# Performance work log

Hardware: AMD Instinct MI355X
Metric: run time of the kernel (lower is better)

Reference implementation:

```python
import jax, jax.numpy as jnp
import numpy as np

DIM = 1024
NUM_EXPERTS = 8
ACTIVE_EXPERTS = 2
EXPERT_DIM = 2048


def setup_inputs() -> dict:
    key = jax.random.key(0)
    k1, k2, k3, k4 = jax.random.split(key, 4)
    x = jax.random.normal(k1, (1, 2048, DIM), dtype=jnp.float32)
    gate_w = jax.random.normal(k2, (NUM_EXPERTS, DIM), dtype=jnp.float32) * 0.02
    balance_bias = jnp.zeros((NUM_EXPERTS,), dtype=jnp.float32)
    w1 = jax.random.normal(k3, (NUM_EXPERTS, EXPERT_DIM, DIM), dtype=jnp.float32) * 0.02
    w2 = jax.random.normal(k4, (NUM_EXPERTS, DIM, EXPERT_DIM), dtype=jnp.float32) * 0.02
    return {"x": x, "gate_w": gate_w, "balance_bias": balance_bias, "w1": w1, "w2": w2}


def reference(x, gate_w, balance_bias, w1, w2):
    B, S, D = x.shape
    T = B * S
    xf = x.reshape(T, D)
    # gating: sigmoid scores with load-balance bias, then top-k
    gate_logits = jnp.einsum('td,ed->te', xf, gate_w)
    gate_scores = jax.nn.sigmoid(gate_logits + balance_bias)
    topk_scores, topk_idx = jax.lax.top_k(gate_scores, ACTIVE_EXPERTS)
    topk_scores = topk_scores / (topk_scores.sum(axis=-1, keepdims=True) + 1e-6)
    # scatter normalized scores into dense combine weights [T, E]
    comb = jnp.zeros((T, NUM_EXPERTS), dtype=x.dtype)
    comb = comb.at[jnp.arange(T)[:, None], topk_idx].add(topk_scores)
    # expert FFNs (dense over experts; combine weight zeroes unselected)
    h = jax.nn.silu(jnp.einsum('td,ehd->teh', xf, w1))   # [T, E, expert_dim]
    expert_out = jnp.einsum('teh,edh->ted', h, w2)        # [T, E, D]
    out = jnp.einsum('te,ted->td', comb, expert_out)
    return out.reshape(B, S, D)
```

## Files before the change

kernel.cpp:

```cpp
#include <hip/hip_runtime.h>

#define T 2048
#define DIM 1024
#define NE 8
#define ED 2048
#define NSLOT (T * 2)
#define KSPLIT 2

#define BM 128
#define BN 128
#define BK 32

typedef __attribute__((ext_vector_type(8))) short s8v;
typedef __attribute__((ext_vector_type(4))) float f32x4;

__device__ __forceinline__ short f2bf(float f) {
    union { float f; unsigned u; } v;
    v.f = f;
    unsigned r = 0x7FFFu + ((v.u >> 16) & 1u);
    v.u += r;
    return (short)(v.u >> 16);
}

__device__ __forceinline__ float bf2f(short s) {
    union { unsigned u; float f; } v;
    v.u = ((unsigned)(unsigned short)s) << 16;
    return v.f;
}

__global__ void router_kernel(const float* __restrict__ x,
                              const float* __restrict__ gw,
                              const float* __restrict__ bias,
                              short* __restrict__ xb,
                              int* __restrict__ counts,
                              int* __restrict__ top2i,
                              float* __restrict__ top2w) {
    int wid = threadIdx.x >> 6;
    int lane = threadIdx.x & 63;
    int t = blockIdx.x * 4 + wid;

    const float* xr = x + (size_t)t * DIM + lane * 16;
    float4 xv[4];
#pragma unroll
    for (int j = 0; j < 4; ++j) xv[j] = *(const float4*)(xr + j * 4);

    s8v o0, o1;
#pragma unroll
    for (int j = 0; j < 2; ++j) {
        o0[j * 4 + 0] = f2bf(xv[j].x); o0[j * 4 + 1] = f2bf(xv[j].y);
        o0[j * 4 + 2] = f2bf(xv[j].z); o0[j * 4 + 3] = f2bf(xv[j].w);
        o1[j * 4 + 0] = f2bf(xv[j + 2].x); o1[j * 4 + 1] = f2bf(xv[j + 2].y);
        o1[j * 4 + 2] = f2bf(xv[j + 2].z); o1[j * 4 + 3] = f2bf(xv[j + 2].w);
    }
    *(s8v*)(xb + (size_t)t * DIM + lane * 16) = o0;
    *(s8v*)(xb + (size_t)t * DIM + lane * 16 + 8) = o1;

    float sc[NE];
#pragma unroll
    for (int e = 0; e < NE; ++e) {
        const float* gr = gw + e * DIM + lane * 16;
        float p = 0.f;
#pragma unroll
        for (int j = 0; j < 4; ++j) {
            float4 g = *(const float4*)(gr + j * 4);
            p += xv[j].x * g.x + xv[j].y * g.y + xv[j].z * g.z + xv[j].w * g.w;
        }
#pragma unroll
        for (int off = 32; off; off >>= 1) p += __shfl_xor(p, off, 64);
        sc[e] = 1.f / (1.f + __expf(-(p + bias[e])));
    }
    int b0 = 0; float s0 = sc[0];
#pragma unroll
    for (int e = 1; e < NE; ++e) if (sc[e] > s0) { s0 = sc[e]; b0 = e; }
    int b1 = -1; float s1 = -1e30f;
#pragma unroll
    for (int e = 0; e < NE; ++e) if (e != b0 && sc[e] > s1) { s1 = sc[e]; b1 = e; }
    float inv = 1.f / (s0 + s1 + 1e-6f);
    if (lane == 0) {
        top2i[t * 2 + 0] = b0; top2i[t * 2 + 1] = b1;
        top2w[t * 2 + 0] = s0 * inv; top2w[t * 2 + 1] = s1 * inv;
        atomicAdd(&counts[b0], 1);
        atomicAdd(&counts[b1], 1);
    }
}

__global__ void prefix_kernel(const int* __restrict__ counts, int* __restrict__ offsets) {
    if (threadIdx.x == 0) {
        int a = 0;
        for (int e = 0; e < NE; ++e) { offsets[e] = a; a += counts[e]; }
    }
}

__global__ void scatter_kernel(const int* __restrict__ top2i,
                               const int* __restrict__ offsets, int* __restrict__ running,
                               int* __restrict__ tok_list, int* __restrict__ slot_of) {
    int t = blockIdx.x * blockDim.x + threadIdx.x;
    if (t >= T) return;
#pragma unroll
    for (int k = 0; k < 2; ++k) {
        int e = top2i[t * 2 + k];
        int pos = atomicAdd(&running[e], 1);
        int slot = offsets[e] + pos;
        tok_list[slot] = t;
        slot_of[t * 2 + k] = slot;
    }
}

__global__ __launch_bounds__(256) void ffn1_kernel(
    const short* __restrict__ xb, const float* __restrict__ w1,
    const int* __restrict__ counts, const int* __restrict__ offsets,
    const int* __restrict__ tok_list, short* __restrict__ h) {
    int e = blockIdx.z;
    int cnt = counts[e];
    int m0 = blockIdx.y * BM;
    if (m0 >= cnt) return;
    int off = offsets[e];
    int n0 = blockIdx.x * BN;

    __shared__ __align__(16) short As[4][BM][8];
    __shared__ __align__(16) short Bs[4][BN][8];

    int tid = threadIdx.x;
    int lane = tid & 63, wid = tid >> 6;
    int mo = (wid >> 1) * 64, no = (wid & 1) * 64;
    int lrow = lane & 15, lq = lane >> 4;

    f32x4 acc[4][4];
#pragma unroll
    for (int mi = 0; mi < 4; ++mi)
#pragma unroll
        for (int ni = 0; ni < 4; ++ni) acc[mi][ni] = (f32x4){0.f, 0.f, 0.f, 0.f};

    int r0 = tid >> 2, q0 = tid & 3;
    int rm0 = m0 + r0;      if (rm0 > cnt - 1) rm0 = cnt - 1;
    int rm1 = m0 + r0 + 64; if (rm1 > cnt - 1) rm1 = cnt - 1;
    int tk0 = tok_list[off + rm0];
    int tk1 = tok_list[off + rm1];
    const short* a0p = xb + (size_t)tk0 * DIM + q0 * 8;
    const short* a1p = xb + (size_t)tk1 * DIM + q0 * 8;
    const float* wb0 = w1 + ((size_t)e * ED + n0 + r0) * DIM + q0 * 8;
    const float* wb1 = wb0 + (size_t)64 * DIM;

    for (int k0 = 0; k0 < DIM; k0 += BK) {
        s8v av0 = *(const s8v*)(a0p + k0);
        s8v av1 = *(const s8v*)(a1p + k0);
        float4 f00 = *(const float4*)(wb0 + k0);
        float4 f01 = *(const float4*)(wb0 + k0 + 4);
        float4 f10 = *(const float4*)(wb1 + k0);
        float4 f11 = *(const float4*)(wb1 + k0 + 4);
        s8v bv0 = { f2bf(f00.x), f2bf(f00.y), f2bf(f00.z), f2bf(f00.w),
                    f2bf(f01.x), f2bf(f01.y), f2bf(f01.z), f2bf(f01.w) };
        s8v bv1 = { f2bf(f10.x), f2bf(f10.y), f2bf(f10.z), f2bf(f10.w),
                    f2bf(f11.x), f2bf(f11.y), f2bf(f11.z), f2bf(f11.w) };
        __syncthreads();
        *(s8v*)&As[q0][r0][0] = av0;
        *(s8v*)&As[q0][r0 + 64][0] = av1;
        *(s8v*)&Bs[q0][r0][0] = bv0;
        *(s8v*)&Bs[q0][r0 + 64][0] = bv1;
        __syncthreads();
        s8v af[4], bf[4];
#pragma unroll
        for (int mi = 0; mi < 4; ++mi) af[mi] = *(const s8v*)&As[lq][mo + mi * 16 + lrow][0];
#pragma unroll
        for (int ni = 0; ni < 4; ++ni) bf[ni] = *(const s8v*)&Bs[lq][no + ni * 16 + lrow][0];
#pragma unroll
        for (int mi = 0; mi < 4; ++mi)
#pragma unroll
            for (int ni = 0; ni < 4; ++ni)
                acc[mi][ni] = __builtin_amdgcn_mfma_f32_16x16x32_bf16(af[mi], bf[ni], acc[mi][ni], 0, 0, 0);
    }

#pragma unroll
    for (int mi = 0; mi < 4; ++mi) {
#pragma unroll
        for (int ni = 0; ni < 4; ++ni) {
            int ln = n0 + no + ni * 16 + lrow;
#pragma unroll
            for (int r = 0; r < 4; ++r) {
                int row = m0 + mo + mi * 16 + lq * 4 + r;
                if (row < cnt) {
                    float v = acc[mi][ni][r];
                    v = v / (1.f + __expf(-v));
                    h[(size_t)(off + row) * ED + ln] = f2bf(v);
                }
            }
        }
    }
}

__global__ __launch_bounds__(256) void ffn2_kernel(
    const short* __restrict__ h, const float* __restrict__ w2,
    const int* __restrict__ counts, const int* __restrict__ offsets,
    short* __restrict__ eo) {
    int z = blockIdx.z;
    int e = z >> 1, ks = z & 1;
    int cnt = counts[e];
    int m0 = blockIdx.y * BM;
    if (m0 >= cnt) return;
    int off = offsets[e];
    int n0 = blockIdx.x * BN;
    const int kbase = ks * (ED / KSPLIT);

    __shared__ __align__(16) short As[4][BM][8];
    __shared__ __align__(16) short Bs[4][BN][8];

    int tid = threadIdx.x;
    int lane = tid & 63, wid = tid >> 6;
    int mo = (wid >> 1) * 64, no = (wid & 1) * 64;
    int lrow = lane & 15, lq = lane >> 4;

    f32x4 acc[4][4];
#pragma unroll
    for (int mi = 0; mi < 4; ++mi)
#pragma unroll
        for (int ni = 0; ni < 4; ++ni) acc[mi][ni] = (f32x4){0.f, 0.f, 0.f, 0.f};

    int r0 = tid >> 2, q0 = tid & 3;
    int rm0 = m0 + r0;      if (rm0 > cnt - 1) rm0 = cnt - 1;
    int rm1 = m0 + r0 + 64; if (rm1 > cnt - 1) rm1 = cnt - 1;
    const short* a0p = h + (size_t)(off + rm0) * ED + q0 * 8;
    const short* a1p = h + (size_t)(off + rm1) * ED + q0 * 8;
    const float* wb0 = w2 + ((size_t)e * DIM + n0 + r0) * ED + q0 * 8;
    const float* wb1 = wb0 + (size_t)64 * ED;

    for (int k0 = kbase; k0 < kbase + ED / KSPLIT; k0 += BK) {
        s8v av0 = *(const s8v*)(a0p + k0);
        s8v av1 = *(const s8v*)(a1p + k0);
        float4 f00 = *(const float4*)(wb0 + k0);
        float4 f01 = *(const float4*)(wb0 + k0 + 4);
        float4 f10 = *(const float4*)(wb1 + k0);
        float4 f11 = *(const float4*)(wb1 + k0 + 4);
        s8v bv0 = { f2bf(f00.x), f2bf(f00.y), f2bf(f00.z), f2bf(f00.w),
                    f2bf(f01.x), f2bf(f01.y), f2bf(f01.z), f2bf(f01.w) };
        s8v bv1 = { f2bf(f10.x), f2bf(f10.y), f2bf(f10.z), f2bf(f10.w),
                    f2bf(f11.x), f2bf(f11.y), f2bf(f11.z), f2bf(f11.w) };
        __syncthreads();
        *(s8v*)&As[q0][r0][0] = av0;
        *(s8v*)&As[q0][r0 + 64][0] = av1;
        *(s8v*)&Bs[q0][r0][0] = bv0;
        *(s8v*)&Bs[q0][r0 + 64][0] = bv1;
        __syncthreads();
        s8v af[4], bf[4];
#pragma unroll
        for (int mi = 0; mi < 4; ++mi) af[mi] = *(const s8v*)&As[lq][mo + mi * 16 + lrow][0];
#pragma unroll
        for (int ni = 0; ni < 4; ++ni) bf[ni] = *(const s8v*)&Bs[lq][no + ni * 16 + lrow][0];
#pragma unroll
        for (int mi = 0; mi < 4; ++mi)
#pragma unroll
            for (int ni = 0; ni < 4; ++ni)
                acc[mi][ni] = __builtin_amdgcn_mfma_f32_16x16x32_bf16(af[mi], bf[ni], acc[mi][ni], 0, 0, 0);
    }

    short* eop = eo + (size_t)ks * NSLOT * DIM;
#pragma unroll
    for (int mi = 0; mi < 4; ++mi) {
#pragma unroll
        for (int ni = 0; ni < 4; ++ni) {
            int ln = n0 + no + ni * 16 + lrow;
#pragma unroll
            for (int r = 0; r < 4; ++r) {
                int row = m0 + mo + mi * 16 + lq * 4 + r;
                if (row < cnt) {
                    eop[(size_t)(off + row) * DIM + ln] = f2bf(acc[mi][ni][r]);
                }
            }
        }
    }
}

__global__ __launch_bounds__(256) void combine_kernel(
    const short* __restrict__ eo, const int* __restrict__ slot_of,
    const float* __restrict__ top2w, float* __restrict__ out) {
    int idx = blockIdx.x * 256 + threadIdx.x;
    int t = idx >> 7;
    int c = idx & 127;
    int s0 = slot_of[2 * t], s1 = slot_of[2 * t + 1];
    float w0 = top2w[2 * t], w1 = top2w[2 * t + 1];
    const short* e0 = eo;
    const short* e1 = eo + (size_t)NSLOT * DIM;
    s8v a0 = *(const s8v*)(e0 + (size_t)s0 * DIM + c * 8);
    s8v a1 = *(const s8v*)(e1 + (size_t)s0 * DIM + c * 8);
    s8v b0 = *(const s8v*)(e0 + (size_t)s1 * DIM + c * 8);
    s8v b1 = *(const s8v*)(e1 + (size_t)s1 * DIM + c * 8);
    float4 o[2];
#pragma unroll
    for (int j = 0; j < 8; ++j) {
        float v = w0 * (bf2f(a0[j]) + bf2f(a1[j])) + w1 * (bf2f(b0[j]) + bf2f(b1[j]));
        ((float*)o)[j] = v;
    }
    float4* op = (float4*)(out + (size_t)t * DIM + c * 8);
    op[0] = o[0];
    op[1] = o[1];
}

extern "C" void kernel_launch(void* const* d_in, const int* in_sizes, int n_in,
                              void* d_out, int out_size, void* d_ws, size_t ws_size,
                              hipStream_t stream) {
    const float* x    = (const float*)d_in[0];
    const float* gw   = (const float*)d_in[1];
    const float* bias = (const float*)d_in[2];
    const float* w1   = (const float*)d_in[3];
    const float* w2   = (const float*)d_in[4];
    float* out = (float*)d_out;

    char* ws = (char*)d_ws;
    short* xb = (short*)ws;
    short* h  = (short*)(ws + (4u << 20));
    short* eo = (short*)(ws + (20u << 20));
    char* meta = ws + (36u << 20);
    int*   counts   = (int*)(meta);
    int*   running  = (int*)(meta + 32);
    int*   offsets  = (int*)(meta + 64);
    int*   tok_list = (int*)(meta + 96);
    int*   slot_of  = (int*)(meta + 96 + 4 * NSLOT);
    int*   top2i    = (int*)(meta + 96 + 8 * NSLOT);
    float* top2w    = (float*)(meta + 96 + 8 * NSLOT + 8 * T);

    hipMemsetAsync(meta, 0, 64, stream);

    router_kernel<<<T / 4, 256, 0, stream>>>(x, gw, bias, xb, counts, top2i, top2w);
    prefix_kernel<<<1, 64, 0, stream>>>(counts, offsets);
    scatter_kernel<<<8, 256, 0, stream>>>(top2i, offsets, running, tok_list, slot_of);
    ffn1_kernel<<<dim3(ED / BN, T / BM, NE), 256, 0, stream>>>(xb, w1, counts, offsets, tok_list, h);
    ffn2_kernel<<<dim3(DIM / BN, T / BM, NE * KSPLIT), 256, 0, stream>>>(h, w2, counts, offsets, eo);
    combine_kernel<<<T * DIM / 8 / 256, 256, 0, stream>>>(eo, slot_of, top2w, out);
}
```

Before: 336.3 us.

## Pre-convert expert weights to bf16 and load GEMM tiles directly into LDS

A new kernel converts w1 and w2 from fp32 to bf16 into workspace at the start of each call. The FFN GEMMs then stream bf16 tiles straight into shared memory with global_load_lds, which removes the per-tile fp32 loads, in-loop conversion and register staging. The prefix and scatter kernels are merged into one single-block plan kernel that uses shared-memory atomics. The trade-off is an extra full pass over both weight tensors, reading fp32 and writing bf16, on every call. The LDS loads are still not double-buffered.

```diff
diff --git a/kernel.cpp b/kernel.cpp
--- a/kernel.cpp
+++ b/kernel.cpp
@@ -6,6 +6,7 @@
 #define ED 2048
 #define NSLOT (T * 2)
 #define KSPLIT 2
+#define WTOT (NE * ED * DIM)
 
 #define BM 128
 #define BN 128
@@ -26,6 +27,30 @@
     union { unsigned u; float f; } v;
     v.u = ((unsigned)(unsigned short)s) << 16;
     return v.f;
+}
+
+__device__ __forceinline__ void glds16(const void* g, void* l) {
+    __builtin_amdgcn_global_load_lds(
+        (const __attribute__((address_space(1))) void*)g,
+        (__attribute__((address_space(3))) void*)l, 16, 0, 0);
+}
+
+__global__ __launch_bounds__(256) void convert_w_kernel(
+    const float* __restrict__ w1, const float* __restrict__ w2,
+    short* __restrict__ w1b, short* __restrict__ w2b) {
+    size_t c = (size_t)blockIdx.x * 256 + threadIdx.x;
+    const float* p1 = w1 + c * 8;
+    const float* p2 = w2 + c * 8;
+    float4 a0 = *(const float4*)(p1);
+    float4 a1 = *(const float4*)(p1 + 4);
+    float4 b0 = *(const float4*)(p2);
+    float4 b1 = *(const float4*)(p2 + 4);
+    s8v o1 = { f2bf(a0.x), f2bf(a0.y), f2bf(a0.z), f2bf(a0.w),
+               f2bf(a1.x), f2bf(a1.y), f2bf(a1.z), f2bf(a1.w) };
+    s8v o2 = { f2bf(b0.x), f2bf(b0.y), f2bf(b0.z), f2bf(b0.w),
+               f2bf(b1.x), f2bf(b1.y), f2bf(b1.z), f2bf(b1.w) };
+    *(s8v*)(w1b + c * 8) = o1;
+    *(s8v*)(w2b + c * 8) = o2;
 }
 
 __global__ void router_kernel(const float* __restrict__ x,
@@ -84,30 +109,30 @@
     }
 }
 
-__global__ void prefix_kernel(const int* __restrict__ counts, int* __restrict__ offsets) {
+__global__ __launch_bounds__(256) void plan_kernel(
+    const int* __restrict__ counts, const int* __restrict__ top2i,
+    int* __restrict__ offsets, int* __restrict__ tok_list, int* __restrict__ slot_of) {
+    __shared__ int soff[NE];
+    __shared__ int srun[NE];
     if (threadIdx.x == 0) {
         int a = 0;
-        for (int e = 0; e < NE; ++e) { offsets[e] = a; a += counts[e]; }
-    }
-}
-
-__global__ void scatter_kernel(const int* __restrict__ top2i,
-                               const int* __restrict__ offsets, int* __restrict__ running,
-                               int* __restrict__ tok_list, int* __restrict__ slot_of) {
-    int t = blockIdx.x * blockDim.x + threadIdx.x;
-    if (t >= T) return;
-#pragma unroll
-    for (int k = 0; k < 2; ++k) {
-        int e = top2i[t * 2 + k];
-        int pos = atomicAdd(&running[e], 1);
-        int slot = offsets[e] + pos;
-        tok_list[slot] = t;
-        slot_of[t * 2 + k] = slot;
+        for (int e = 0; e < NE; ++e) { soff[e] = a; offsets[e] = a; a += counts[e]; srun[e] = 0; }
+    }
+    __syncthreads();
+    for (int t = threadIdx.x; t < T; t += 256) {
+#pragma unroll
+        for (int k = 0; k < 2; ++k) {
+            int e = top2i[t * 2 + k];
+            int pos = atomicAdd(&srun[e], 1);
+            int slot = soff[e] + pos;
+            tok_list[slot] = t;
+            slot_of[t * 2 + k] = slot;
+        }
     }
 }
 
 __global__ __launch_bounds__(256) void ffn1_kernel(
-    const short* __restrict__ xb, const float* __restrict__ w1,
+    const short* __restrict__ xb, const short* __restrict__ w1b,
     const int* __restrict__ counts, const int* __restrict__ offsets,
     const int* __restrict__ tok_list, short* __restrict__ h) {
     int e = blockIdx.z;
@@ -121,8 +146,8 @@
     __shared__ __align__(16) short Bs[4][BN][8];
 
     int tid = threadIdx.x;
-    int lane = tid & 63, wid = tid >> 6;
-    int mo = (wid >> 1) * 64, no = (wid & 1) * 64;
+    int lane = tid & 63, w = tid >> 6;
+    int mo = (w >> 1) * 64, no = (w & 1) * 64;
     int lrow = lane & 15, lq = lane >> 4;
 
     f32x4 acc[4][4];
@@ -131,32 +156,23 @@
 #pragma unroll
         for (int ni = 0; ni < 4; ++ni) acc[mi][ni] = (f32x4){0.f, 0.f, 0.f, 0.f};
 
-    int r0 = tid >> 2, q0 = tid & 3;
-    int rm0 = m0 + r0;      if (rm0 > cnt - 1) rm0 = cnt - 1;
-    int rm1 = m0 + r0 + 64; if (rm1 > cnt - 1) rm1 = cnt - 1;
-    int tk0 = tok_list[off + rm0];
-    int tk1 = tok_list[off + rm1];
-    const short* a0p = xb + (size_t)tk0 * DIM + q0 * 8;
-    const short* a1p = xb + (size_t)tk1 * DIM + q0 * 8;
-    const float* wb0 = w1 + ((size_t)e * ED + n0 + r0) * DIM + q0 * 8;
-    const float* wb1 = wb0 + (size_t)64 * DIM;
+    int ra0 = m0 + lane;      if (ra0 > cnt - 1) ra0 = cnt - 1;
+    int ra1 = m0 + 64 + lane; if (ra1 > cnt - 1) ra1 = cnt - 1;
+    const short* a0 = xb + (size_t)tok_list[off + ra0] * DIM + w * 8;
+    const short* a1 = xb + (size_t)tok_list[off + ra1] * DIM + w * 8;
+    const short* b0 = w1b + ((size_t)e * ED + n0 + lane) * DIM + w * 8;
+    const short* b1 = b0 + (size_t)64 * DIM;
+    short* lA0 = &As[w][0][0];
+    short* lA1 = &As[w][64][0];
+    short* lB0 = &Bs[w][0][0];
+    short* lB1 = &Bs[w][64][0];
 
     for (int k0 = 0; k0 < DIM; k0 += BK) {
-        s8v av0 = *(const s8v*)(a0p + k0);
-        s8v av1 = *(const s8v*)(a1p + k0);
-        float4 f00 = *(const float4*)(wb0 + k0);
-        float4 f01 = *(const float4*)(wb0 + k0 + 4);
-        float4 f10 = *(const float4*)(wb1 + k0);
-        float4 f11 = *(const float4*)(wb1 + k0 + 4);
-        s8v bv0 = { f2bf(f00.x), f2bf(f00.y), f2bf(f00.z), f2bf(f00.w),
-                    f2bf(f01.x), f2bf(f01.y), f2bf(f01.z), f2bf(f01.w) };
-        s8v bv1 = { f2bf(f10.x), f2bf(f10.y), f2bf(f10.z), f2bf(f10.w),
-                    f2bf(f11.x), f2bf(f11.y), f2bf(f11.z), f2bf(f11.w) };
         __syncthreads();
-        *(s8v*)&As[q0][r0][0] = av0;
-        *(s8v*)&As[q0][r0 + 64][0] = av1;
-        *(s8v*)&Bs[q0][r0][0] = bv0;
-        *(s8v*)&Bs[q0][r0 + 64][0] = bv1;
+        glds16(a0 + k0, lA0);
+        glds16(a1 + k0, lA1);
+        glds16(b0 + k0, lB0);
+        glds16(b1 + k0, lB1);
         __syncthreads();
         s8v af[4], bf[4];
 #pragma unroll
@@ -189,7 +205,7 @@
 }
 
 __global__ __launch_bounds__(256) void ffn2_kernel(
-    const short* __restrict__ h, const float* __restrict__ w2,
+    const short* __restrict__ h, const short* __restrict__ w2b,
     const int* __restrict__ counts, const int* __restrict__ offsets,
     short* __restrict__ eo) {
     int z = blockIdx.z;
@@ -205,8 +221,8 @@
     __shared__ __align__(16) short Bs[4][BN][8];
 
     int tid = threadIdx.x;
-    int lane = tid & 63, wid = tid >> 6;
-    int mo = (wid >> 1) * 64, no = (wid & 1) * 64;
+    int lane = tid & 63, w = tid >> 6;
+    int mo = (w >> 1) * 64, no = (w & 1) * 64;
     int lrow = lane & 15, lq = lane >> 4;
 
     f32x4 acc[4][4];
@@ -215,30 +231,23 @@
 #pragma unroll
         for (int ni = 0; ni < 4; ++ni) acc[mi][ni] = (f32x4){0.f, 0.f, 0.f, 0.f};
 
-    int r0 = tid >> 2, q0 = tid & 3;
-    int rm0 = m0 + r0;      if (rm0 > cnt - 1) rm0 = cnt - 1;
-    int rm1 = m0 + r0 + 64; if (rm1 > cnt - 1) rm1 = cnt - 1;
-    const short* a0p = h + (size_t)(off + rm0) * ED + q0 * 8;
-    const short* a1p = h + (size_t)(off + rm1) * ED + q0 * 8;
-    const float* wb0 = w2 + ((size_t)e * DIM + n0 + r0) * ED + q0 * 8;
-    const float* wb1 = wb0 + (size_t)64 * ED;
-
-    for (int k0 = kbase; k0 < kbase + ED / KSPLIT; k0 += BK) {
-        s8v av0 = *(const s8v*)(a0p + k0);
-        s8v av1 = *(const s8v*)(a1p + k0);
-        float4 f00 = *(const float4*)(wb0 + k0);
-        float4 f01 = *(const float4*)(wb0 + k0 + 4);
-        float4 f10 = *(const float4*)(wb1 + k0);
-        float4 f11 = *(const float4*)(wb1 + k0 + 4);
-        s8v bv0 = { f2bf(f00.x), f2bf(f00.y), f2bf(f00.z), f2bf(f00.w),
-                    f2bf(f01.x), f2bf(f01.y), f2bf(f01.z), f2bf(f01.w) };
-        s8v bv1 = { f2bf(f10.x), f2bf(f10.y), f2bf(f10.z), f2bf(f10.w),
-                    f2bf(f11.x), f2bf(f11.y), f2bf(f11.z), f2bf(f11.w) };
+    int ra0 = m0 + lane;      if (ra0 > cnt - 1) ra0 = cnt - 1;
+    int ra1 = m0 + 64 + lane; if (ra1 > cnt - 1) ra1 = cnt - 1;
+    const short* a0 = h + (size_t)(off + ra0) * ED + kbase + w * 8;
+    const short* a1 = h + (size_t)(off + ra1) * ED + kbase + w * 8;
+    const short* b0 = w2b + ((size_t)e * DIM + n0 + lane) * ED + kbase + w * 8;
+    const short* b1 = b0 + (size_t)64 * ED;
+    short* lA0 = &As[w][0][0];
+    short* lA1 = &As[w][64][0];
+    short* lB0 = &Bs[w][0][0];
+    short* lB1 = &Bs[w][64][0];
+
+    for (int k0 = 0; k0 < ED / KSPLIT; k0 += BK) {
         __syncthreads();
-        *(s8v*)&As[q0][r0][0] = av0;
-        *(s8v*)&As[q0][r0 + 64][0] = av1;
-        *(s8v*)&Bs[q0][r0][0] = bv0;
-        *(s8v*)&Bs[q0][r0 + 64][0] = bv1;
+        glds16(a0 + k0, lA0);
+        glds16(a1 + k0, lA1);
+        glds16(b0 + k0, lB0);
+        glds16(b1 + k0, lB1);
         __syncthreads();
         s8v af[4], bf[4];
 #pragma unroll
@@ -305,24 +314,25 @@
     float* out = (float*)d_out;
 
     char* ws = (char*)d_ws;
-    short* xb = (short*)ws;
-    short* h  = (short*)(ws + (4u << 20));
-    short* eo = (short*)(ws + (20u << 20));
-    char* meta = ws + (36u << 20);
+    short* xb  = (short*)ws;
+    short* h   = (short*)(ws + (4ull << 20));
+    short* w1b = (short*)(ws + (20ull << 20));
+    short* eo  = (short*)(ws + (20ull << 20));
+    short* w2b = (short*)(ws + (52ull << 20));
+    char* meta = ws + (84ull << 20);
     int*   counts   = (int*)(meta);
-    int*   running  = (int*)(meta + 32);
     int*   offsets  = (int*)(meta + 64);
-    int*   tok_list = (int*)(meta + 96);
-    int*   slot_of  = (int*)(meta + 96 + 4 * NSLOT);
-    int*   top2i    = (int*)(meta + 96 + 8 * NSLOT);
-    float* top2w    = (float*)(meta + 96 + 8 * NSLOT + 8 * T);
-
-    hipMemsetAsync(meta, 0, 64, stream);
-
+    int*   tok_list = (int*)(meta + 128);
+    int*   slot_of  = (int*)(meta + 128 + 4 * NSLOT);
+    int*   top2i    = (int*)(meta + 128 + 8 * NSLOT);
+    float* top2w    = (float*)(meta + 128 + 8 * NSLOT + 8 * T);
+
+    hipMemsetAsync(counts, 0, 32, stream);
+
+    convert_w_kernel<<<WTOT / 8 / 256, 256, 0, stream>>>(w1, w2, w1b, w2b);
     router_kernel<<<T / 4, 256, 0, stream>>>(x, gw, bias, xb, counts, top2i, top2w);
-    prefix_kernel<<<1, 64, 0, stream>>>(counts, offsets);
-    scatter_kernel<<<8, 256, 0, stream>>>(top2i, offsets, running, tok_list, slot_of);
-    ffn1_kernel<<<dim3(ED / BN, T / BM, NE), 256, 0, stream>>>(xb, w1, counts, offsets, tok_list, h);
-    ffn2_kernel<<<dim3(DIM / BN, T / BM, NE * KSPLIT), 256, 0, stream>>>(h, w2, counts, offsets, eo);
+    plan_kernel<<<1, 256, 0, stream>>>(counts, top2i, offsets, tok_list, slot_of);
+    ffn1_kernel<<<dim3(ED / BN, T / BM, NE), 256, 0, stream>>>(xb, w1b, counts, offsets, tok_list, h);
+    ffn2_kernel<<<dim3(DIM / BN, T / BM, NE * KSPLIT), 256, 0, stream>>>(h, w2b, counts, offsets, eo);
     combine_kernel<<<T * DIM / 8 / 256, 256, 0, stream>>>(eo, slot_of, top2w, out);
 }
```

After: 337.7 us. Within noise of the previous version (+0.4%).
